# Kernel tuning notes

Hardware: AMD Instinct MI355X
Metric: run time of the kernel (lower is better)

## Reference

```python
import math
import jax, jax.numpy as jnp
import numpy as np

B, S, DIM, H = 16, 1024, 1024, 16
HD = DIM // H            # head_dim = 64
ROPE_DIM = HD // 2       # 32; per-axis rotary dim
FT = 32                  # ft_seq_len, FT*FT == S
PT = 16                  # pt_seq_len
THETA = 10000.0
EPS = 1e-6


def _rope_cos_sin():
    # freqs_for='lang'
    freqs = 1.0 / THETA ** (jnp.arange(0, ROPE_DIM, 2, dtype=jnp.float32) / ROPE_DIM)  # [ROPE_DIM//2]
    t = jnp.arange(FT, dtype=jnp.float32) / FT * PT                                    # [FT]
    fs = jnp.einsum('n,f->nf', t, freqs)                                               # [FT, ROPE_DIM//2]
    fs = jnp.repeat(fs, 2, axis=-1)                                                    # [FT, ROPE_DIM]
    fh = jnp.broadcast_to(fs[:, None, :], (FT, FT, ROPE_DIM))
    fw = jnp.broadcast_to(fs[None, :, :], (FT, FT, ROPE_DIM))
    f = jnp.concatenate([fh, fw], axis=-1).reshape(-1, 2 * ROPE_DIM)                   # [S, HD]
    return jnp.cos(f), jnp.sin(f)


def _rotate_half(x):
    x1, x2 = jnp.split(x, 2, axis=-1)
    return jnp.concatenate((-x2, x1), axis=-1)


def _rms_norm(x, w):
    xf = x.astype(jnp.float32)
    var = jnp.mean(jnp.square(xf), axis=-1, keepdims=True)
    return (w * (xf * jax.lax.rsqrt(var + EPS))).astype(x.dtype)


def setup_inputs() -> dict:
    key = jax.random.key(0)
    ks = jax.random.split(key, 4)
    sd = 1.0 / math.sqrt(DIM)
    return {
        'x': jax.random.normal(ks[0], (B, S, DIM), dtype=jnp.float32),
        'w_qkv': jax.random.normal(ks[1], (DIM, 3 * DIM), dtype=jnp.float32) * sd,
        'b_qkv': jnp.zeros((3 * DIM,), dtype=jnp.float32),
        'q_norm_w': jnp.ones((HD,), dtype=jnp.float32),
        'k_norm_w': jnp.ones((HD,), dtype=jnp.float32),
        'w_out': jax.random.normal(ks[2], (DIM, DIM), dtype=jnp.float32) * sd,
        'b_out': jnp.zeros((DIM,), dtype=jnp.float32),
    }


def reference(x, w_qkv, b_qkv, q_norm_w, k_norm_w, w_out, b_out):
    cos, sin = _rope_cos_sin()                    # [S, HD] each
    cos = cos[None, None].astype(x.dtype)
    sin = sin[None, None].astype(x.dtype)

    qkv = x @ w_qkv + b_qkv                       # [B,S,3*DIM]
    qkv = qkv.reshape(B, S, 3, H, HD).transpose(2, 0, 3, 1, 4)  # [3,B,H,S,HD]
    q, k, v = qkv[0], qkv[1], qkv[2]

    q = _rms_norm(q, q_norm_w)
    k = _rms_norm(k, k_norm_w)

    q = q * cos + _rotate_half(q) * sin
    k = k * cos + _rotate_half(k) * sin

    scale = 1.0 / math.sqrt(HD)
    logits = jnp.einsum('bhqd,bhkd->bhqk', q.astype(jnp.float32), k.astype(jnp.float32)) * scale
    attn = jax.nn.softmax(logits, axis=-1).astype(x.dtype)
    out = jnp.einsum('bhqk,bhkd->bhqd', attn, v)  # [B,H,S,HD]

    out = out.transpose(0, 2, 1, 3).reshape(B, S, DIM)
    return out @ w_out + b_out
```

## Files before the change

kernel.cpp:

```cpp
#include <hip/hip_runtime.h>
#include <cstdint>
#include <cstddef>

#define B_    16
#define S_    1024
#define DIM_  1024
#define H_    16
#define HD_   64
#define TDIM  3072

typedef unsigned short ushort_t;
typedef unsigned int   uint_t;
typedef __attribute__((ext_vector_type(8)))  short s8v;
typedef __attribute__((ext_vector_type(4)))  float f32x4;
typedef __attribute__((ext_vector_type(16))) float f32x16;

__device__ __forceinline__ float b2f(ushort_t u) {
    union { uint_t i; float f; } t; t.i = (uint_t)u << 16; return t.f;
}
__device__ __forceinline__ ushort_t f2b(float f) {
    union { float f; uint_t i; } t; t.f = f;
    uint_t r = t.i + 0x7FFFu + ((t.i >> 16) & 1u);
    return (ushort_t)(r >> 16);
}
__device__ __forceinline__ uint_t cvt_pk_bf16(float a, float b) {
    uint_t r;
    asm("v_cvt_pk_bf16_f32 %0, %1, %2" : "=v"(r) : "v"(a), "v"(b));
    return r;
}
__device__ __forceinline__ float max3f(float a, float b, float c) {
    float r;
    asm("v_max3_f32 %0, %1, %2, %3" : "=v"(r) : "v"(a), "v"(b), "v"(c));
    return r;
}

__device__ __forceinline__ f32x4 mfma_bf16(s8v a, s8v b, f32x4 c) {
    asm volatile("v_mfma_f32_16x16x32_bf16 %0, %1, %2, %0" : "+v"(c) : "v"(a), "v"(b));
    return c;
}
__device__ __forceinline__ f32x16 mfma32_bf16(s8v a, s8v b, f32x16 c) {
    asm volatile("v_mfma_f32_32x32x16_bf16 %0, %1, %2, %0" : "+v"(c) : "v"(a), "v"(b));
    return c;
}

__device__ __forceinline__ void gload16(const void* g, void* l) {
    __builtin_amdgcn_global_load_lds(
        (const __attribute__((address_space(1))) uint_t*)g,
        (__attribute__((address_space(3))) uint_t*)l, 16, 0, 0);
}

__device__ __forceinline__ void bar() {
    asm volatile("" ::: "memory");
    __builtin_amdgcn_s_barrier();
    asm volatile("" ::: "memory");
}
__device__ __forceinline__ void wait_vm0() {
    asm volatile("s_waitcnt vmcnt(0)" ::: "memory");
}
__device__ __forceinline__ void wait_vm4() {
    asm volatile("s_waitcnt vmcnt(4)" ::: "memory");
}

__global__ __launch_bounds__(256) void f32_to_bf16_vec(const float* __restrict__ src,
                                                       short* __restrict__ dst, int n8) {
    int i = blockIdx.x * 256 + threadIdx.x;
    if (i < n8) {
        float4 a = *(const float4*)(src + (size_t)i * 8);
        float4 b = *(const float4*)(src + (size_t)i * 8 + 4);
        s8v t;
        t[0] = (short)f2b(a.x); t[1] = (short)f2b(a.y);
        t[2] = (short)f2b(a.z); t[3] = (short)f2b(a.w);
        t[4] = (short)f2b(b.x); t[5] = (short)f2b(b.y);
        t[6] = (short)f2b(b.z); t[7] = (short)f2b(b.w);
        *(s8v*)(dst + (size_t)i * 8) = t;
    }
}

__global__ __launch_bounds__(256) void rope_tables(float* __restrict__ cos_t,
                                                   float* __restrict__ sin_t) {
    int idx = blockIdx.x * 256 + threadIdx.x;
    int s = idx >> 6;
    int d = idx & 63;
    int pos = (d < 32) ? (s >> 5) : (s & 31);
    int i   = (d & 31) >> 1;
    float freq  = expf(-(float)i * 0.5756462732485115f);
    float angle = (float)pos * 0.5f * freq;
    cos_t[idx] = cosf(angle);
    sin_t[idx] = sinf(angle);
}

__global__ __launch_bounds__(256) void transpose_to_bf16(const float* __restrict__ Wsrc,
                                                         short* __restrict__ WT,
                                                         int K, int N) {
    __shared__ float t[32][33];
    int tx = threadIdx.x & 31, ty = threadIdx.x >> 5;
    int n0 = blockIdx.x * 32, k0 = blockIdx.y * 32;
#pragma unroll
    for (int i = 0; i < 4; ++i)
        t[ty + 8 * i][tx] = Wsrc[(size_t)(k0 + ty + 8 * i) * N + n0 + tx];
    __syncthreads();
#pragma unroll
    for (int i = 0; i < 4; ++i)
        WT[(size_t)(n0 + ty + 8 * i) * K + k0 + tx] = (short)f2b(t[tx][ty + 8 * i]);
}

template<typename CT, bool NORM>
__global__ __launch_bounds__(512, 2) void gemm8ph(
        const short* __restrict__ A, const short* __restrict__ BT,
        const float* __restrict__ bias, CT* __restrict__ C,
        int M, int N, int K, int NX,
        const float* __restrict__ qw, const float* __restrict__ kw,
        const float* __restrict__ cos_t, const float* __restrict__ sin_t) {
    __shared__ short As[2][256 * 64];
    __shared__ short Bs[3][256 * 64];

    const int tid  = threadIdx.x;
    const int w    = tid >> 6;
    const int lane = tid & 63;
    const int l15  = lane & 15, lg = lane >> 4;
    const int wm = w >> 2, wn = w & 3;

    const int nwg  = gridDim.x;
    const int cpx  = nwg >> 3;
    const int wgid = (blockIdx.x & 7) * cpx + (blockIdx.x >> 3);
    const int bx = wgid % NX, by = wgid / NX;
    const int m0 = by * 256, n0 = bx * 256;

    const int NT = K >> 6;

    const int sgrow = w * 8 + (lane >> 3);
    const int ksrc  = (((lane & 7) ^ (lane >> 3)) * 8);

    auto stageA = [&](int t, int buf) {
        const size_t k0 = (size_t)t * 64;
#pragma unroll
        for (int j = 0; j < 4; ++j)
            gload16(A + (size_t)(m0 + j * 64 + sgrow) * K + k0 + ksrc,
                    &As[buf][(j * 64 + w * 8) * 64]);
    };
    auto stageB = [&](int t, int buf) {
        const size_t k0 = (size_t)t * 64;
#pragma unroll
        for (int j = 0; j < 4; ++j)
            gload16(BT + (size_t)(n0 + j * 64 + sgrow) * K + k0 + ksrc,
                    &Bs[buf][(j * 64 + w * 8) * 64]);
    };

    stageA(0, 0);
    stageB(0, 0);
    stageB(1, 1);
    wait_vm4();
    bar();

    f32x4 acc[8][4] = {};
    s8v a_f[4][2];
    s8v b_f[4][2];

    const int swz = l15 & 7;

    int bufB = 0;
    for (int t = 0; t < NT; ++t) {
        const int bufA = t & 1;
        const int nbufB = (bufB == 2) ? 0 : bufB + 1;
        const int sbufB = (nbufB == 2) ? 0 : nbufB + 1;

#pragma unroll
        for (int i = 0; i < 4; ++i) {
            int row = wm * 128 + i * 16 + l15;
#pragma unroll
            for (int kk = 0; kk < 2; ++kk)
                a_f[i][kk] = *(const s8v*)&As[bufA][row * 64 + (((kk * 4 + lg) ^ swz) * 8)];
        }
#pragma unroll
        for (int ni = 0; ni < 2; ++ni) {
            int row = wn * 64 + ni * 16 + l15;
#pragma unroll
            for (int kk = 0; kk < 2; ++kk)
                b_f[ni][kk] = *(const s8v*)&Bs[bufB][row * 64 + (((kk * 4 + lg) ^ swz) * 8)];
        }
        if (t + 1 < NT) stageA(t + 1, bufA ^ 1);
        bar();
        __builtin_amdgcn_s_setprio(1);
#pragma unroll
        for (int i = 0; i < 4; ++i)
#pragma unroll
            for (int ni = 0; ni < 2; ++ni)
#pragma unroll
                for (int kk = 0; kk < 2; ++kk)
                    acc[i][ni] = mfma_bf16(a_f[i][kk], b_f[ni][kk], acc[i][ni]);
        __builtin_amdgcn_s_setprio(0);
        bar();

#pragma unroll
        for (int ni = 2; ni < 4; ++ni) {
            int row = wn * 64 + ni * 16 + l15;
#pragma unroll
            for (int kk = 0; kk < 2; ++kk)
                b_f[ni][kk] = *(const s8v*)&Bs[bufB][row * 64 + (((kk * 4 + lg) ^ swz) * 8)];
        }
        if (t + 2 < NT) stageB(t + 2, sbufB);
        bar();
        __builtin_amdgcn_s_setprio(1);
#pragma unroll
        for (int i = 0; i < 4; ++i)
#pragma unroll
            for (int ni = 2; ni < 4; ++ni)
#pragma unroll
                for (int kk = 0; kk < 2; ++kk)
                    acc[i][ni] = mfma_bf16(a_f[i][kk], b_f[ni][kk], acc[i][ni]);
        __builtin_amdgcn_s_setprio(0);
        bar();

#pragma unroll
        for (int i = 0; i < 4; ++i) {
            int row = wm * 128 + 64 + i * 16 + l15;
#pragma unroll
            for (int kk = 0; kk < 2; ++kk)
                a_f[i][kk] = *(const s8v*)&As[bufA][row * 64 + (((kk * 4 + lg) ^ swz) * 8)];
        }
        bar();
        __builtin_amdgcn_s_setprio(1);
#pragma unroll
        for (int i = 0; i < 4; ++i)
#pragma unroll
            for (int ni = 0; ni < 2; ++ni)
#pragma unroll
                for (int kk = 0; kk < 2; ++kk)
                    acc[4 + i][ni] = mfma_bf16(a_f[i][kk], b_f[ni][kk], acc[4 + i][ni]);
        __builtin_amdgcn_s_setprio(0);
        bar();

        __builtin_amdgcn_s_setprio(1);
#pragma unroll
        for (int i = 0; i < 4; ++i)
#pragma unroll
            for (int ni = 2; ni < 4; ++ni)
#pragma unroll
                for (int kk = 0; kk < 2; ++kk)
                    acc[4 + i][ni] = mfma_bf16(a_f[i][kk], b_f[ni][kk], acc[4 + i][ni]);
        __builtin_amdgcn_s_setprio(0);
        if (t < NT - 2) wait_vm4();
        else            wait_vm0();
        bar();
        bufB = nbufB;
    }

    const int colbase = n0 + wn * 64;
    if constexpr (NORM) {
        if (colbase < 2048) {
            const float* nw = (colbase < 1024) ? qw : kw;
            float wv[4], bv[4];
#pragma unroll
            for (int ni = 0; ni < 4; ++ni) {
                wv[ni] = nw[16 * ni + l15];
                bv[ni] = bias[colbase + 16 * ni + l15];
            }
#pragma unroll
            for (int mi = 0; mi < 8; ++mi) {
#pragma unroll
                for (int r = 0; r < 4; ++r) {
                    int row = m0 + wm * 128 + mi * 16 + lg * 4 + r;
                    int s = row & (S_ - 1);
                    float v[4];
#pragma unroll
                    for (int ni = 0; ni < 4; ++ni) v[ni] = acc[mi][ni][r] + bv[ni];
                    float ss = v[0]*v[0] + v[1]*v[1] + v[2]*v[2] + v[3]*v[3];
                    ss += __shfl_xor(ss, 1);
                    ss += __shfl_xor(ss, 2);
                    ss += __shfl_xor(ss, 4);
                    ss += __shfl_xor(ss, 8);
                    float rms = rsqrtf(ss * (1.0f / 64.0f) + 1e-6f);
                    float xn[4];
#pragma unroll
                    for (int ni = 0; ni < 4; ++ni) xn[ni] = v[ni] * rms * wv[ni];
#pragma unroll
                    for (int ni = 0; ni < 4; ++ni) {
                        int d = 16 * ni + l15;
                        float c  = cos_t[s * 64 + d];
                        float sn = sin_t[s * 64 + d];
                        float rot = (ni < 2) ? -xn[ni + 2] : xn[ni - 2];
                        C[(size_t)row * N + colbase + d] = (short)f2b(xn[ni] * c + rot * sn);
                    }
                }
            }
            return;
        }
    }
#pragma unroll
    for (int ni = 0; ni < 4; ++ni) {
        float bvv = bias[colbase + 16 * ni + l15];
#pragma unroll
        for (int mi = 0; mi < 8; ++mi) {
#pragma unroll
            for (int r = 0; r < 4; ++r) {
                size_t row = (size_t)(m0 + wm * 128 + mi * 16 + lg * 4 + r);
                int    col = colbase + 16 * ni + l15;
                float v = acc[mi][ni][r] + bvv;
                if constexpr (sizeof(CT) == 4) C[row * N + col] = v;
                else                           C[row * N + col] = (short)f2b(v);
            }
        }
    }
}

__global__ __launch_bounds__(256) void attn_mfma(const short* __restrict__ qkv,
                                                 short* __restrict__ attn) {
    __shared__ ushort_t pool[9216];
    ushort_t* Ks = pool;
    ushort_t* Vt = pool + 4608;

    const float SC  = 0.18033688011112042f;
    const float THR = 11.0f;

    const int tid  = threadIdx.x;
    const int w    = tid >> 6;
    const int lane = tid & 63;
    const int l31  = lane & 31, l5 = lane >> 5;

    const int bid = blockIdx.x;
    const int xcd = bid & 7;
    const int jj_ = bid >> 3;
    const int bh  = xcd * 32 + (jj_ & 31);
    const int b   = bh >> 4, h = bh & 15;
    const int q0  = (jj_ >> 5) * 128;

    const short* qbase = qkv + (size_t)b * S_ * TDIM + h * HD_;
    const short* kb_ = qbase + DIM_;
    const short* vb_ = qbase + 2 * DIM_;

    s8v qf[4];
#pragma unroll
    for (int kc = 0; kc < 4; ++kc)
        qf[kc] = *(const s8v*)(qbase + (size_t)(q0 + w * 32 + l31) * TDIM + kc * 16 + l5 * 8);

    f32x16 of0 = {}, of1 = {};
    float m_s = -1e30f, l_s = 0.f;

    const int kr   = tid >> 3;
    const int kp8  = (tid & 7) * 8;
    const int vkp  = tid >> 3;
    const int va   = tid & 7;
    const int vp8  = va * 8;
    const int k2    = 2 * vkp;
    const int kperm = (k2 & 0x33) | ((k2 & 4) << 1) | ((k2 & 8) >> 1);
    const int vcol  = kperm ^ ((va & 3) << 4);
    const int vsw   = ((l31 >> 3) & 3) << 4;

    s8v kA, kB, vA, vB;
    auto prefetch = [&](int kt) {
        const short* kbt = kb_ + (size_t)kt * 64 * TDIM;
        const short* vbt = vb_ + (size_t)kt * 64 * TDIM;
        kA = *(const s8v*)(kbt + (size_t)kr * TDIM + kp8);
        kB = *(const s8v*)(kbt + (size_t)(kr + 32) * TDIM + kp8);
        vA = *(const s8v*)(vbt + (size_t)k2 * TDIM + vp8);
        vB = *(const s8v*)(vbt + (size_t)(k2 + 1) * TDIM + vp8);
    };
    prefetch(0);

    for (int kt = 0; kt < 16; ++kt) {
        *(s8v*)&Ks[kr * 72 + kp8]        = kA;
        *(s8v*)&Ks[(kr + 32) * 72 + kp8] = kB;
#pragma unroll
        for (int j = 0; j < 8; ++j) {
            uint_t pk = (ushort_t)vA[j] | ((uint_t)(ushort_t)vB[j] << 16);
            *(uint_t*)&Vt[(vp8 + j) * 72 + vcol] = pk;
        }
        __syncthreads();

        if (kt < 15) prefetch(kt + 1);

        f32x16 st0 = {}, st1 = {};
        __builtin_amdgcn_s_setprio(1);
#pragma unroll
        for (int kc = 0; kc < 4; ++kc) {
            s8v kf0 = *(const s8v*)&Ks[l31 * 72 + kc * 16 + l5 * 8];
            s8v kf1 = *(const s8v*)&Ks[(32 + l31) * 72 + kc * 16 + l5 * 8];
            st0 = mfma32_bf16(kf0, qf[kc], st0);
            st1 = mfma32_bf16(kf1, qf[kc], st1);
        }
        __builtin_amdgcn_s_setprio(0);

        float ma = fmaxf(st0[0], st1[0]);
        float mb = fmaxf(st0[8], st1[8]);
#pragma unroll
        for (int r = 1; r < 8; ++r) {
            ma = max3f(st0[r],     st1[r],     ma);
            mb = max3f(st0[8 + r], st1[8 + r], mb);
        }
        float mx = fmaxf(ma, mb);
        mx = fmaxf(mx, __shfl_xor(mx, 32));
        float mxs = mx * SC;

        if (!__all(mxs <= m_s + THR)) {
            float mnew  = fmaxf(m_s, mxs);
            float alpha = exp2f(m_s - mnew);
            m_s = mnew;
            l_s *= alpha;
#pragma unroll
            for (int r = 0; r < 16; ++r) { of0[r] *= alpha; of1[r] *= alpha; }
        }

        float la = 0.f, lb = 0.f, lc = 0.f, ld = 0.f;
#pragma unroll
        for (int r = 0; r < 16; r += 2) {
            float p00 = exp2f(__builtin_fmaf(st0[r],     SC, -m_s));
            float p01 = exp2f(__builtin_fmaf(st0[r + 1], SC, -m_s));
            float p10 = exp2f(__builtin_fmaf(st1[r],     SC, -m_s));
            float p11 = exp2f(__builtin_fmaf(st1[r + 1], SC, -m_s));
            st0[r] = p00; st0[r + 1] = p01;
            st1[r] = p10; st1[r + 1] = p11;
            la += p00; lb += p01; lc += p10; ld += p11;
        }
        float ls = (la + lb) + (lc + ld);
        ls += __shfl_xor(ls, 32);
        l_s += ls;

        uint_t P20[8], P21[8];
#pragma unroll
        for (int i = 0; i < 8; ++i) {
            P20[i] = cvt_pk_bf16(st0[2 * i], st0[2 * i + 1]);
            P21[i] = cvt_pk_bf16(st1[2 * i], st1[2 * i + 1]);
        }

        __builtin_amdgcn_s_setprio(1);
#pragma unroll
        for (int kb = 0; kb < 2; ++kb) {
            const uint_t* P2 = kb ? P21 : P20;
#pragma unroll
            for (int c = 0; c < 2; ++c) {
                union { uint_t u[4]; s8v v; } pf;
                pf.u[0] = P2[4 * c + 0];
                pf.u[1] = P2[4 * c + 1];
                pf.u[2] = P2[4 * c + 2];
                pf.u[3] = P2[4 * c + 3];

                int kcol = (kb * 32 + c * 16 + l5 * 8) ^ vsw;
                s8v vf0 = *(const s8v*)&Vt[l31 * 72 + kcol];
                s8v vf1 = *(const s8v*)&Vt[(32 + l31) * 72 + kcol];
                of0 = mfma32_bf16(vf0, pf.v, of0);
                of1 = mfma32_bf16(vf1, pf.v, of1);
            }
        }
        __builtin_amdgcn_s_setprio(0);
        __syncthreads();
    }

    float inv = 1.0f / l_s;
    ushort_t* OL = pool + w * 2304;
#pragma unroll
    for (int r = 0; r < 16; ++r) {
        int d = (r & 3) + 8 * (r >> 2) + 4 * l5;
        OL[l31 * 72 + d]      = f2b(of0[r] * inv);
        OL[l31 * 72 + 32 + d] = f2b(of1[r] * inv);
    }
#pragma unroll
    for (int i = 0; i < 4; ++i) {
        int idx = lane + i * 64;
        int row = idx >> 3, ch = idx & 7;
        *(s8v*)&attn[((size_t)b * S_ + q0 + w * 32 + row) * DIM_ + h * HD_ + ch * 8] =
            *(const s8v*)&OL[row * 72 + ch * 8];
    }
}

extern "C" void kernel_launch(void* const* d_in, const int* in_sizes, int n_in,
                              void* d_out, int out_size, void* d_ws, size_t ws_size,
                              hipStream_t stream) {
    const float* x        = (const float*)d_in[0];
    const float* w_qkv    = (const float*)d_in[1];
    const float* b_qkv    = (const float*)d_in[2];
    const float* q_norm_w = (const float*)d_in[3];
    const float* k_norm_w = (const float*)d_in[4];
    const float* w_out    = (const float*)d_in[5];
    const float* b_out    = (const float*)d_in[6];
    float* out = (float*)d_out;

    const size_t OFF_QKV = 0;
    const size_t OFF_ATT = 100663296;
    const size_t OFF_XB  = OFF_ATT + 33554432;
    const size_t OFF_WQ  = OFF_XB + 33554432;
    const size_t OFF_WO  = OFF_WQ + 6291456;
    const size_t OFF_CT  = OFF_WO + 2097152;
    const size_t OFF_ST  = OFF_CT + 262144;
    const size_t NEED    = OFF_ST + 262144;

    if (ws_size < NEED) {
        hipMemsetAsync(d_out, 0, (size_t)out_size * sizeof(float), stream);
        return;
    }

    char* ws = (char*)d_ws;
    short* qkv   = (short*)(ws + OFF_QKV);
    short* attnb = (short*)(ws + OFF_ATT);
    short* xb    = (short*)(ws + OFF_XB);
    short* wqkvT = (short*)(ws + OFF_WQ);
    short* woutT = (short*)(ws + OFF_WO);
    float* cos_t = (float*)(ws + OFF_CT);
    float* sin_t = (float*)(ws + OFF_ST);

    rope_tables<<<dim3(256), dim3(256), 0, stream>>>(cos_t, sin_t);
    f32_to_bf16_vec<<<dim3(8192), dim3(256), 0, stream>>>(x, xb, 2097152);
    transpose_to_bf16<<<dim3(96, 32), dim3(256), 0, stream>>>(w_qkv, wqkvT, 1024, 3072);
    transpose_to_bf16<<<dim3(32, 32), dim3(256), 0, stream>>>(w_out, woutT, 1024, 1024);

    gemm8ph<short, true><<<dim3(768), dim3(512), 0, stream>>>(
        xb, wqkvT, b_qkv, qkv, 16384, 3072, 1024, 12,
        q_norm_w, k_norm_w, cos_t, sin_t);

    attn_mfma<<<dim3(2048), dim3(256), 0, stream>>>(qkv, attnb);

    gemm8ph<float, false><<<dim3(256), dim3(512), 0, stream>>>(
        attnb, woutT, b_out, out, 16384, 1024, 1024, 4,
        nullptr, nullptr, nullptr, nullptr);
}
```

Before: 307.9 us.

## Register double-buffer GEMM fragments and cut per-iteration barriers to one

Restructures the GEMM main loop so the LDS fragment reads for the next k-tile are issued during the last MFMA block of the current tile, with both A halves held in separate registers. The five barriers per iteration become one, and the global stage loads for A and B are issued together at the top of the loop. Launch bounds drop the min-2-blocks hint, which lets the compiler use more registers but may lower occupancy. There is a risk of an LDS hazard: the buffer being overwritten by the next stageA/stageB must no longer be read by any wave when only one barrier is kept.

```diff
diff --git a/kernel.cpp b/kernel.cpp
--- a/kernel.cpp
+++ b/kernel.cpp
@@ -105,7 +105,7 @@
 }
 
 template<typename CT, bool NORM>
-__global__ __launch_bounds__(512, 2) void gemm8ph(
+__global__ __launch_bounds__(512) void gemm8ph(
         const short* __restrict__ A, const short* __restrict__ BT,
         const float* __restrict__ bias, CT* __restrict__ C,
         int M, int N, int K, int NX,
@@ -146,102 +146,102 @@
                     &Bs[buf][(j * 64 + w * 8) * 64]);
     };
 
+    const int swz = l15 & 7;
+
+    auto rdA = [&](int buf, int mh, s8v (&dst)[4][2]) {
+#pragma unroll
+        for (int i = 0; i < 4; ++i) {
+            int row = wm * 128 + mh * 64 + i * 16 + l15;
+#pragma unroll
+            for (int kk = 0; kk < 2; ++kk)
+                dst[i][kk] = *(const s8v*)&As[buf][row * 64 + (((kk * 4 + lg) ^ swz) * 8)];
+        }
+    };
+    auto rdB = [&](int buf, int nh, s8v (&dst)[4][2]) {
+#pragma unroll
+        for (int ni = 0; ni < 2; ++ni) {
+            int row = wn * 64 + (nh * 2 + ni) * 16 + l15;
+#pragma unroll
+            for (int kk = 0; kk < 2; ++kk)
+                dst[nh * 2 + ni][kk] = *(const s8v*)&Bs[buf][row * 64 + (((kk * 4 + lg) ^ swz) * 8)];
+        }
+    };
+
     stageA(0, 0);
     stageB(0, 0);
     stageB(1, 1);
     wait_vm4();
     bar();
 
+    s8v a0[4][2], a1[4][2], bb[4][2];
+    rdA(0, 0, a0);
+    rdB(0, 0, bb);
+    rdB(0, 1, bb);
+    rdA(0, 1, a1);
+
     f32x4 acc[8][4] = {};
-    s8v a_f[4][2];
-    s8v b_f[4][2];
-
-    const int swz = l15 & 7;
 
     int bufB = 0;
     for (int t = 0; t < NT; ++t) {
-        const int bufA = t & 1;
+        const int bufA  = t & 1;
         const int nbufB = (bufB == 2) ? 0 : bufB + 1;
         const int sbufB = (nbufB == 2) ? 0 : nbufB + 1;
 
-#pragma unroll
-        for (int i = 0; i < 4; ++i) {
-            int row = wm * 128 + i * 16 + l15;
-#pragma unroll
-            for (int kk = 0; kk < 2; ++kk)
-                a_f[i][kk] = *(const s8v*)&As[bufA][row * 64 + (((kk * 4 + lg) ^ swz) * 8)];
-        }
-#pragma unroll
-        for (int ni = 0; ni < 2; ++ni) {
-            int row = wn * 64 + ni * 16 + l15;
-#pragma unroll
-            for (int kk = 0; kk < 2; ++kk)
-                b_f[ni][kk] = *(const s8v*)&Bs[bufB][row * 64 + (((kk * 4 + lg) ^ swz) * 8)];
-        }
         if (t + 1 < NT) stageA(t + 1, bufA ^ 1);
+        if (t + 2 < NT) stageB(t + 2, sbufB);
+
+        __builtin_amdgcn_s_setprio(1);
+#pragma unroll
+        for (int i = 0; i < 4; ++i)
+#pragma unroll
+            for (int ni = 0; ni < 2; ++ni)
+#pragma unroll
+                for (int kk = 0; kk < 2; ++kk)
+                    acc[i][ni] = mfma_bf16(a0[i][kk], bb[ni][kk], acc[i][ni]);
+        __builtin_amdgcn_s_setprio(0);
+
+        __builtin_amdgcn_s_setprio(1);
+#pragma unroll
+        for (int i = 0; i < 4; ++i)
+#pragma unroll
+            for (int ni = 2; ni < 4; ++ni)
+#pragma unroll
+                for (int kk = 0; kk < 2; ++kk)
+                    acc[i][ni] = mfma_bf16(a0[i][kk], bb[ni][kk], acc[i][ni]);
+        __builtin_amdgcn_s_setprio(0);
+
+        __builtin_amdgcn_s_setprio(1);
+#pragma unroll
+        for (int i = 0; i < 4; ++i)
+#pragma unroll
+            for (int ni = 0; ni < 2; ++ni)
+#pragma unroll
+                for (int kk = 0; kk < 2; ++kk)
+                    acc[4 + i][ni] = mfma_bf16(a1[i][kk], bb[ni][kk], acc[4 + i][ni]);
+        __builtin_amdgcn_s_setprio(0);
+
+        if (t < NT - 2) wait_vm4(); else wait_vm0();
         bar();
+
+        if (t + 1 < NT) {
+            rdA(bufA ^ 1, 0, a0);
+            rdB(nbufB, 0, bb);
+        }
+
         __builtin_amdgcn_s_setprio(1);
 #pragma unroll
         for (int i = 0; i < 4; ++i)
 #pragma unroll
-            for (int ni = 0; ni < 2; ++ni)
+            for (int ni = 2; ni < 4; ++ni)
 #pragma unroll
                 for (int kk = 0; kk < 2; ++kk)
-                    acc[i][ni] = mfma_bf16(a_f[i][kk], b_f[ni][kk], acc[i][ni]);
+                    acc[4 + i][ni] = mfma_bf16(a1[i][kk], bb[ni][kk], acc[4 + i][ni]);
         __builtin_amdgcn_s_setprio(0);
-        bar();
-
-#pragma unroll
-        for (int ni = 2; ni < 4; ++ni) {
-            int row = wn * 64 + ni * 16 + l15;
-#pragma unroll
-            for (int kk = 0; kk < 2; ++kk)
-                b_f[ni][kk] = *(const s8v*)&Bs[bufB][row * 64 + (((kk * 4 + lg) ^ swz) * 8)];
-        }
-        if (t + 2 < NT) stageB(t + 2, sbufB);
-        bar();
-        __builtin_amdgcn_s_setprio(1);
-#pragma unroll
-        for (int i = 0; i < 4; ++i)
-#pragma unroll
-            for (int ni = 2; ni < 4; ++ni)
-#pragma unroll
-                for (int kk = 0; kk < 2; ++kk)
-                    acc[i][ni] = mfma_bf16(a_f[i][kk], b_f[ni][kk], acc[i][ni]);
-        __builtin_amdgcn_s_setprio(0);
-        bar();
-
-#pragma unroll
-        for (int i = 0; i < 4; ++i) {
-            int row = wm * 128 + 64 + i * 16 + l15;
-#pragma unroll
-            for (int kk = 0; kk < 2; ++kk)
-                a_f[i][kk] = *(const s8v*)&As[bufA][row * 64 + (((kk * 4 + lg) ^ swz) * 8)];
-        }
-        bar();
-        __builtin_amdgcn_s_setprio(1);
-#pragma unroll
-        for (int i = 0; i < 4; ++i)
-#pragma unroll
-            for (int ni = 0; ni < 2; ++ni)
-#pragma unroll
-                for (int kk = 0; kk < 2; ++kk)
-                    acc[4 + i][ni] = mfma_bf16(a_f[i][kk], b_f[ni][kk], acc[4 + i][ni]);
-        __builtin_amdgcn_s_setprio(0);
-        bar();
-
-        __builtin_amdgcn_s_setprio(1);
-#pragma unroll
-        for (int i = 0; i < 4; ++i)
-#pragma unroll
-            for (int ni = 2; ni < 4; ++ni)
-#pragma unroll
-                for (int kk = 0; kk < 2; ++kk)
-                    acc[4 + i][ni] = mfma_bf16(a_f[i][kk], b_f[ni][kk], acc[4 + i][ni]);
-        __builtin_amdgcn_s_setprio(0);
-        if (t < NT - 2) wait_vm4();
-        else            wait_vm0();
-        bar();
+
+        if (t + 1 < NT) {
+            rdB(nbufB, 1, bb);
+            rdA(bufA ^ 1, 1, a1);
+        }
         bufB = nbufB;
     }
 
```

After: 296.5 us. -3.7%, faster.
